# Kernel optimization log

Measured on AMD Instinct MI355X. Metric: run time of the kernel, lower is better.

The kernel has to match this reference:

```python
import jax, jax.numpy as jnp
import numpy as np

DIM = 64
B_GRAPHS = 16
N_NODES = 4096
N_EDGES = 16384
SLOPE = 0.01  # PyTorch leaky_relu default negative slope


def lrelu(x):
    return jnp.where(x >= 0, x, SLOPE * x)


def setup_inputs() -> dict:
    key = jax.random.key(0)
    ks = jax.random.split(key, 16)
    d = DIM

    def rn(k, shape, scale=0.05):
        return jax.random.normal(k, shape, dtype=jnp.float32) * scale

    def z(*s):
        return jnp.zeros(s, jnp.float32)

    return {
        "x": jax.random.normal(ks[0], (N_NODES, 3), dtype=jnp.float32),
        "edge_attr": jax.random.normal(ks[1], (N_EDGES, 4), dtype=jnp.float32),
        "edge_index": jax.random.randint(ks[2], (2, N_EDGES), 0, N_NODES),
        "batch": jnp.sort(jax.random.randint(ks[3], (N_NODES,), 0, B_GRAPHS)),
        # lin0
        "W0": rn(ks[4], (3, d)), "b0": z(d),
        # edge MLP: Linear(4,d) -> LeakyReLU -> Linear(d, d*d)
        "We1": rn(ks[5], (4, d)), "be1": z(d),
        "We2": rn(ks[6], (d, d * d), 0.01), "be2": z(d * d),
        # NNConv root weight + bias
        "root": rn(ks[7], (d, d)), "conv_b": z(d),
        # GRU(d, d)  (PyTorch layout: [3d, in] / [3d, hid], gate order r,z,n)
        "Wih": rn(ks[8], (3 * d, d)), "Whh": rn(ks[9], (3 * d, d)),
        "bih": z(3 * d), "bhh": z(3 * d),
        # Set2Set LSTM(2d, d)  (gate order i,f,g,o)
        "lWih": rn(ks[10], (4 * d, 2 * d)), "lWhh": rn(ks[11], (4 * d, d)),
        "lbih": z(4 * d), "lbhh": z(4 * d),
        # lin_out: Linear(2d, 2)
        "Wout": rn(ks[12], (2 * d, 2)), "bout": z(2),
    }


def _forward(x, edge_attr, W0, b0, We1, be1, We2, be2, root, conv_b,
             Wih, Whh, bih, bhh, lWih, lWhh, lbih, lbhh, Wout, bout,
             edge_index, batch):
    d = DIM
    N = x.shape[0]
    E = edge_attr.shape[0]
    src, dst = edge_index[0], edge_index[1]  # messages flow src(j) -> dst(i)

    out = lrelu(x @ W0 + b0)  # [N, d]
    h = out                    # GRU hidden state (h = out.unsqueeze(0))

    # Edge-conditioned weights: constant across the 6 iterations, compute once.
    he = lrelu(edge_attr @ We1 + be1)          # [E, d]
    W_e = (he @ We2 + be2).reshape(E, d, d)    # [E, d, d]
    deg = jax.ops.segment_sum(jnp.ones((E,), jnp.float32), dst, num_segments=N)
    inv_deg = (1.0 / jnp.maximum(deg, 1.0))[:, None]  # mean aggr, clamp like PyG

    for _ in range(6):
        # NNConv: gather x_j, per-edge matmul, scatter-mean, plus root term
        msg = jnp.einsum('ed,edf->ef', out[src], W_e)            # [E, d]
        agg = jax.ops.segment_sum(msg, dst, num_segments=N) * inv_deg
        m = lrelu(agg + out @ root + conv_b)                     # [N, d]
        # GRU cell (single step, PyTorch gate order r, z, n)
        gi = m @ Wih.T + bih
        gh = h @ Whh.T + bhh
        i_r, i_z, i_n = jnp.split(gi, 3, axis=-1)
        h_r, h_z, h_n = jnp.split(gh, 3, axis=-1)
        r = jax.nn.sigmoid(i_r + h_r)
        zg = jax.nn.sigmoid(i_z + h_z)
        n = jnp.tanh(i_n + r * h_n)
        h = (1.0 - zg) * n + zg * h
        out = h

    # Set2Set pooling, processing_steps = 1
    Bg = B_GRAPHS
    q_star = jnp.zeros((Bg, 2 * d), jnp.float32)
    hl = jnp.zeros((Bg, d), jnp.float32)
    cl = jnp.zeros((Bg, d), jnp.float32)
    gates = q_star @ lWih.T + lbih + hl @ lWhh.T + lbhh
    gi_, gf_, gg_, go_ = jnp.split(gates, 4, axis=-1)
    cl = jax.nn.sigmoid(gf_) * cl + jax.nn.sigmoid(gi_) * jnp.tanh(gg_)
    q = jax.nn.sigmoid(go_) * jnp.tanh(cl)         # [Bg, d]
    e = jnp.sum(out * q[batch], axis=-1)           # [N]
    emax = jax.ops.segment_max(e, batch, num_segments=Bg)
    a = jnp.exp(e - emax[batch])
    asum = jax.ops.segment_sum(a, batch, num_segments=Bg)
    a = a / asum[batch]                            # per-graph softmax attention
    rpool = jax.ops.segment_sum(a[:, None] * out, batch, num_segments=Bg)
    q_star = jnp.concatenate([q, rpool], axis=-1)  # [Bg, 2d]

    return q_star @ Wout + bout                    # [Bg, 2]


def reference(x, edge_attr, edge_index, batch, W0, b0, We1, be1, We2, be2,
              root, conv_b, Wih, Whh, bih, bhh, lWih, lWhh, lbih, lbhh,
              Wout, bout):
    return _forward(x, edge_attr, W0, b0, We1, be1, We2, be2, root, conv_b,
                    Wih, Whh, bih, bhh, lWih, lWhh, lbih, lbhh, Wout, bout,
                    edge_index, batch)
```

## Files before the change

kernel.cpp:

```cpp
#include <hip/hip_runtime.h>
#include <cstddef>

#define NE 16384
#define NN 4096
#define BG 16
#define NT 16
#define ACH 8

__device__ __forceinline__ float lrelu(float v){ return v >= 0.f ? v : 0.01f*v; }
__device__ __forceinline__ float sigm(float v){ return 1.f/(1.f + expf(-v)); }

__global__ __launch_bounds__(256) void setup_kernel(
    const float* __restrict__ x, const float* __restrict__ ea,
    const int* __restrict__ ei,
    const float* __restrict__ W0, const float* __restrict__ b0,
    const float* __restrict__ We1, const float* __restrict__ be1,
    const float* __restrict__ Wih, const float* __restrict__ Whh,
    float* __restrict__ W8T,
    float* __restrict__ h, float* __restrict__ he,
    int* __restrict__ deg, int* __restrict__ cnt)
{
    int t = blockIdx.x*256 + threadIdx.x;
    {
        int e = t >> 6, f = t & 63;
        float v = be1[f];
        #pragma unroll
        for (int d = 0; d < 4; ++d) v += ea[e*4+d]*We1[d*64+f];
        he[t] = lrelu(v);
    }
    if (t < NN*64) {
        int n = t >> 6, f = t & 63;
        float v = b0[f];
        #pragma unroll
        for (int d = 0; d < 3; ++d) v += x[n*3+d]*W0[d*64+f];
        h[t] = lrelu(v);
    }
    if (t < 32768) {
        int k = t >> 9, g = (t >> 3) & 63, j = t & 7;
        float v = 0.f;
        if (j < 3)      v = Wih[(j*64+g)*64 + k];
        else if (j < 6) v = Whh[((j-3)*64+g)*64 + k];
        W8T[t] = v;
    }
    if (t < NE) {
        atomicAdd(&deg[ei[NE + t]], 1);
        atomicAdd(&cnt[ei[t]], 1);
    }
}

__global__ __launch_bounds__(256) void scan_kernel(const int* __restrict__ cnt,
                                                   int* __restrict__ offs)
{
    __shared__ int ps[256];
    int t = threadIdx.x;
    int base = t*16;
    int loc[16];
    int s = 0;
    #pragma unroll
    for (int i = 0; i < 16; ++i) { loc[i] = s; s += cnt[base+i]; }
    ps[t] = s; __syncthreads();
    for (int off = 1; off < 256; off <<= 1) {
        int v = 0;
        if (t >= off) v = ps[t-off];
        __syncthreads();
        if (t >= off) ps[t] += v;
        __syncthreads();
    }
    int pre = (t == 0) ? 0 : ps[t-1];
    #pragma unroll
    for (int i = 0; i < 16; ++i) offs[base+i] = pre + loc[i];
    if (t == 255) offs[NN] = pre + s;
}

__global__ __launch_bounds__(256) void scatter_kernel(
    const int* __restrict__ ei, const int* __restrict__ offs,
    int* __restrict__ cnt,
    int* __restrict__ srcs, int* __restrict__ dsts, int* __restrict__ perm)
{
    int e = blockIdx.x*256 + threadIdx.x;
    if (e >= NE) return;
    int s = ei[e], d = ei[NE + e];
    int old = atomicSub(&cnt[s], 1);
    int pos = offs[s] + old - 1;
    srcs[pos] = s; dsts[pos] = d; perm[pos] = e;
}

__global__ __launch_bounds__(256) void reorder_kernel(
    const float* __restrict__ he, const int* __restrict__ perm,
    float* __restrict__ he_srt)
{
    int t = blockIdx.x*256 + threadIdx.x;
    he_srt[t] = he[(size_t)perm[t>>6]*64 + (t & 63)];
}

__global__ __launch_bounds__(256) void inv_range_kernel(
    const int* __restrict__ deg, const int* __restrict__ batch,
    float* __restrict__ inv_deg, int* __restrict__ gstart, int* __restrict__ gend)
{
    int n = blockIdx.x*256 + threadIdx.x;
    if (n >= NN) return;
    inv_deg[n] = 1.f / fmaxf((float)deg[n], 1.f);
    int b  = batch[n];
    int bp = (n == 0)    ? -1 : batch[n-1];
    int bn = (n == NN-1) ? BG : batch[n+1];
    for (int g = bp+1; g <= b; ++g) gstart[g] = n;
    for (int g = b;   g <  bn; ++g) gend[g]   = n+1;
    if (n == 0)    for (int g = 0;   g < b;  ++g) gend[g]   = 0;
    if (n == NN-1) for (int g = b+1; g < BG; ++g) gstart[g] = NN;
}

__global__ __launch_bounds__(1024) void conv_kernel(
    const float* __restrict__ h, const float* __restrict__ We2,
    const float* __restrict__ be2, const float* __restrict__ he_srt,
    const int* __restrict__ offs, const int* __restrict__ srcs,
    const int* __restrict__ dsts, float* __restrict__ agg)
{
    __shared__ float hsT[64][NT];
    __shared__ float Tb [NT][64];
    __shared__ float Tc [2][ACH][NT][64];
    __shared__ float he_s[2][128][ACH];
    int t  = threadIdx.x;
    int n0 = blockIdx.x * NT;

    { int n = t >> 6, i = t & 63; hsT[i][n] = h[(size_t)(n0+n)*64 + i]; }
    int ebase = offs[n0];
    int ecnt  = offs[n0+NT] - ebase;
    int eend  = ebase + ecnt;
    __syncthreads();

    int aT = t >> 6;
    int nT = ((t >> 4) & 3) * 4;
    int fT = (t & 15) * 4;
    int ct   = t - 512;
    int slot = ct >> 4;
    int f4   = (ct & 15) * 4;
    int nl0=-1,dt0=0,nl1=-1,dt1=0,nl2=-1,dt2=0,nl3=-1,dt3=0;
    float4 m0={0,0,0,0},m1={0,0,0,0},m2={0,0,0,0},m3={0,0,0,0};
    if (t >= 512) {
        if (slot      < ecnt) { nl0 = srcs[ebase+slot]    - n0; dt0 = dsts[ebase+slot];    }
        if (slot + 32 < ecnt) { nl1 = srcs[ebase+slot+32] - n0; dt1 = dsts[ebase+slot+32]; }
        if (slot + 64 < ecnt) { nl2 = srcs[ebase+slot+64] - n0; dt2 = dsts[ebase+slot+64]; }
        if (slot + 96 < ecnt) { nl3 = srcs[ebase+slot+96] - n0; dt3 = dsts[ebase+slot+96]; }
    }

#define EDGE_ACC(mj, nlj, row, buf_) \
    if (nlj >= 0) { \
        float4 hA = *(const float4*)&he_s[buf_][row][0]; \
        float4 hB = *(const float4*)&he_s[buf_][row][4]; \
        float4 t0 = *(const float4*)&Tc[buf_][0][nlj][f4]; \
        float4 t1 = *(const float4*)&Tc[buf_][1][nlj][f4]; \
        float4 t2 = *(const float4*)&Tc[buf_][2][nlj][f4]; \
        float4 t3 = *(const float4*)&Tc[buf_][3][nlj][f4]; \
        float4 t4 = *(const float4*)&Tc[buf_][4][nlj][f4]; \
        float4 t5 = *(const float4*)&Tc[buf_][5][nlj][f4]; \
        float4 t6 = *(const float4*)&Tc[buf_][6][nlj][f4]; \
        float4 t7 = *(const float4*)&Tc[buf_][7][nlj][f4]; \
        mj.x += hA.x*t0.x+hA.y*t1.x+hA.z*t2.x+hA.w*t3.x+hB.x*t4.x+hB.y*t5.x+hB.z*t6.x+hB.w*t7.x; \
        mj.y += hA.x*t0.y+hA.y*t1.y+hA.z*t2.y+hA.w*t3.y+hB.x*t4.y+hB.y*t5.y+hB.z*t6.y+hB.w*t7.y; \
        mj.z += hA.x*t0.z+hA.y*t1.z+hA.z*t2.z+hA.w*t3.z+hB.x*t4.z+hB.y*t5.z+hB.z*t6.z+hB.w*t7.z; \
        mj.w += hA.x*t0.w+hA.y*t1.w+hA.z*t2.w+hA.w*t3.w+hB.x*t4.w+hB.y*t5.w+hB.z*t6.w+hB.w*t7.w; \
    }

#define CONSUME(cm) { \
    int buf_ = (cm) & 1; \
    EDGE_ACC(m0, nl0, (slot),      buf_) \
    EDGE_ACC(m1, nl1, (slot+32),   buf_) \
    EDGE_ACC(m2, nl2, (slot+64),   buf_) \
    EDGE_ACC(m3, nl3, (slot+96),   buf_) \
    for (int e = ebase + 128 + slot; e < eend; e += 32) { \
        int nl = srcs[e] - n0, dtv = dsts[e]; \
        const float* hep = he_srt + (size_t)e*64 + (cm)*ACH; \
        float4 pm = {0,0,0,0}; \
        _Pragma("unroll") \
        for (int a = 0; a < ACH; ++a) { \
            float hv = hep[a]; \
            float4 tv = *(const float4*)&Tc[buf_][a][nl][f4]; \
            pm.x += hv*tv.x; pm.y += hv*tv.y; pm.z += hv*tv.z; pm.w += hv*tv.w; \
        } \
        if ((cm) == 0) { \
            float4 b = *(const float4*)&Tb[nl][f4]; \
            pm.x += b.x; pm.y += b.y; pm.z += b.z; pm.w += b.w; \
        } \
        float* ap = agg + (size_t)dtv*64 + f4; \
        atomicAdd(ap+0, pm.x); atomicAdd(ap+1, pm.y); \
        atomicAdd(ap+2, pm.z); atomicAdd(ap+3, pm.w); \
    } \
}

    for (int c = 0; c < 8; ++c) {
        if (t < 512) {
            const float* Wp = We2 + (size_t)(c*ACH + aT)*4096 + fT;
            float4 A0={0,0,0,0},A1={0,0,0,0},A2={0,0,0,0},A3={0,0,0,0};
            #pragma unroll 8
            for (int i = 0; i < 64; ++i) {
                float4 w  = *(const float4*)(Wp + (size_t)i*64);
                float4 hv = *(const float4*)&hsT[i][nT];
                A0.x += hv.x*w.x; A0.y += hv.x*w.y; A0.z += hv.x*w.z; A0.w += hv.x*w.w;
                A1.x += hv.y*w.x; A1.y += hv.y*w.y; A1.z += hv.y*w.z; A1.w += hv.y*w.w;
                A2.x += hv.z*w.x; A2.y += hv.z*w.y; A2.z += hv.z*w.z; A2.w += hv.z*w.w;
                A3.x += hv.w*w.x; A3.y += hv.w*w.y; A3.z += hv.w*w.z; A3.w += hv.w*w.w;
            }
            int buf = c & 1;
            *(float4*)&Tc[buf][aT][nT+0][fT] = A0;
            *(float4*)&Tc[buf][aT][nT+1][fT] = A1;
            *(float4*)&Tc[buf][aT][nT+2][fT] = A2;
            *(float4*)&Tc[buf][aT][nT+3][fT] = A3;
            if (c == 0) {
                #pragma unroll
                for (int r = 0; r < 2; ++r) {
                    int idx = t + r*512;
                    int n = idx >> 6, f = idx & 63;
                    float acc = 0.f;
                    #pragma unroll 8
                    for (int i = 0; i < 64; ++i) acc += hsT[i][n]*be2[i*64+f];
                    Tb[n][f] = acc;
                }
            }
        } else {
            {
                int le = ct >> 2, a2 = (ct & 3) * 2;
                if (ebase + le < NE)
                    *(float2*)&he_s[c&1][le][a2] =
                        *(const float2*)&he_srt[(size_t)(ebase+le)*64 + c*ACH + a2];
            }
            if (c >= 1) CONSUME(c-1);
        }
        __syncthreads();
    }
    if (t >= 512) {
        CONSUME(7);
        if (nl0 >= 0) {
            float4 b = *(const float4*)&Tb[nl0][f4];
            float* ap = agg + (size_t)dt0*64 + f4;
            atomicAdd(ap+0, m0.x+b.x); atomicAdd(ap+1, m0.y+b.y);
            atomicAdd(ap+2, m0.z+b.z); atomicAdd(ap+3, m0.w+b.w);
        }
        if (nl1 >= 0) {
            float4 b = *(const float4*)&Tb[nl1][f4];
            float* ap = agg + (size_t)dt1*64 + f4;
            atomicAdd(ap+0, m1.x+b.x); atomicAdd(ap+1, m1.y+b.y);
            atomicAdd(ap+2, m1.z+b.z); atomicAdd(ap+3, m1.w+b.w);
        }
        if (nl2 >= 0) {
            float4 b = *(const float4*)&Tb[nl2][f4];
            float* ap = agg + (size_t)dt2*64 + f4;
            atomicAdd(ap+0, m2.x+b.x); atomicAdd(ap+1, m2.y+b.y);
            atomicAdd(ap+2, m2.z+b.z); atomicAdd(ap+3, m2.w+b.w);
        }
        if (nl3 >= 0) {
            float4 b = *(const float4*)&Tb[nl3][f4];
            float* ap = agg + (size_t)dt3*64 + f4;
            atomicAdd(ap+0, m3.x+b.x); atomicAdd(ap+1, m3.y+b.y);
            atomicAdd(ap+2, m3.z+b.z); atomicAdd(ap+3, m3.w+b.w);
        }
    }
#undef CONSUME
#undef EDGE_ACC
}

__global__ __launch_bounds__(512) void node_kernel(
    const float* __restrict__ W8T, const float* __restrict__ root,
    const float* __restrict__ conv_b, const float* __restrict__ inv_deg,
    const float* __restrict__ bih, const float* __restrict__ bhh,
    float* __restrict__ h, float* __restrict__ agg)
{
    __shared__ float hs[8][64];
    __shared__ float ms[8][64];
    int t = threadIdx.x;
    int n = t >> 6, g = t & 63;
    int gn = blockIdx.x*8 + n;
    hs[n][g] = h[(size_t)gn*64 + g];
    __syncthreads();
    {
        size_t ix = (size_t)gn*64 + g;
        float v = agg[ix]*inv_deg[gn] + conv_b[g];
        agg[ix] = 0.f;
        #pragma unroll 8
        for (int k = 0; k < 64; ++k) v += hs[n][k]*root[k*64 + g];
        ms[n][g] = lrelu(v);
    }
    __syncthreads();

    float ir=0.f, iz=0.f, in_=0.f, hr=0.f, hz=0.f, hn=0.f;
    const float* Wp = W8T + (size_t)g*8;
    #pragma unroll 8
    for (int k = 0; k < 64; ++k) {
        float am = ms[n][k], ah = hs[n][k];
        float4 w0 = *(const float4*)(Wp + (size_t)k*512);
        float4 w1 = *(const float4*)(Wp + (size_t)k*512 + 4);
        ir  += am*w0.x; iz += am*w0.y; in_ += am*w0.z;
        hr  += ah*w0.w; hz += ah*w1.x; hn  += ah*w1.y;
    }
    float r  = sigm(ir + bih[g]      + hr + bhh[g]);
    float z  = sigm(iz + bih[64+g]   + hz + bhh[64+g]);
    float nn = tanhf(in_ + bih[128+g] + r*(hn + bhh[128+g]));
    h[(size_t)gn*64 + g] = (1.f - z)*nn + z*hs[n][g];
}

__device__ __forceinline__ float q_val(const float* lbih, const float* lbhh, int g)
{
    float gi = lbih[g]     + lbhh[g];
    float gg = lbih[128+g] + lbhh[128+g];
    float go = lbih[192+g] + lbhh[192+g];
    return sigm(go)*tanhf(sigm(gi)*tanhf(gg));
}

__global__ __launch_bounds__(256) void e_kernel(
    const float* __restrict__ h, const float* __restrict__ lbih,
    const float* __restrict__ lbhh, float* __restrict__ e)
{
    __shared__ float qs[64];
    int t = threadIdx.x;
    if (t < 64) qs[t] = q_val(lbih, lbhh, t);
    __syncthreads();
    int w = t >> 6, f = t & 63;
    int n = blockIdx.x*4 + w;
    float p = h[(size_t)n*64 + f]*qs[f];
    #pragma unroll
    for (int off = 32; off; off >>= 1) p += __shfl_xor(p, off);
    if (f == 0) e[n] = p;
}

__global__ __launch_bounds__(1024) void pool_kernel(
    const float* __restrict__ h, float* __restrict__ e,
    const int* __restrict__ gstart, const int* __restrict__ gend,
    const float* __restrict__ lbih, const float* __restrict__ lbhh,
    const float* __restrict__ Wout, const float* __restrict__ bout,
    float* __restrict__ out)
{
    __shared__ float red[1024];
    __shared__ float rp[64];
    __shared__ float sval;
    int g = blockIdx.x, t = threadIdx.x;
    int s = gstart[g], en = gend[g];

    float mx = -1e30f;
    for (int n = s+t; n < en; n += 1024) mx = fmaxf(mx, e[n]);
    red[t] = mx; __syncthreads();
    for (int st = 512; st; st >>= 1) { if (t < st) red[t] = fmaxf(red[t], red[t+st]); __syncthreads(); }
    if (t == 0) sval = red[0];
    __syncthreads();
    float lmx = sval;
    __syncthreads();

    float sm = 0.f;
    for (int n = s+t; n < en; n += 1024) { float a = expf(e[n]-lmx); e[n] = a; sm += a; }
    red[t] = sm; __syncthreads();
    for (int st = 512; st; st >>= 1) { if (t < st) red[t] += red[t+st]; __syncthreads(); }
    if (t == 0) sval = (red[0] > 0.f) ? 1.f/red[0] : 0.f;
    __syncthreads();
    float inv_asum = sval;
    __syncthreads();

    int w = t >> 6, f = t & 63;
    float racc = 0.f;
    for (int n = s+w; n < en; n += 16) racc += e[n]*h[(size_t)n*64 + f];
    red[t] = racc; __syncthreads();
    if (w == 0) {
        float a = 0.f;
        #pragma unroll
        for (int i = 0; i < 16; ++i) a += red[i*64 + f];
        rp[f] = a*inv_asum;
    }
    __syncthreads();

    if (t < 64) {
        float qv = q_val(lbih, lbhh, t);
        float p0 = qv*Wout[t*2]   + rp[t]*Wout[(64+t)*2];
        float p1 = qv*Wout[t*2+1] + rp[t]*Wout[(64+t)*2+1];
        #pragma unroll
        for (int off = 32; off; off >>= 1) { p0 += __shfl_xor(p0, off); p1 += __shfl_xor(p1, off); }
        if (t == 0) { out[g*2] = p0 + bout[0]; out[g*2+1] = p1 + bout[1]; }
    }
}

extern "C" void kernel_launch(void* const* d_in, const int* in_sizes, int n_in,
                              void* d_out, int out_size, void* d_ws, size_t ws_size,
                              hipStream_t stream)
{
    const float* x      = (const float*)d_in[0];
    const float* ea     = (const float*)d_in[1];
    const int*   ei     = (const int*)  d_in[2];
    const int*   batch  = (const int*)  d_in[3];
    const float* W0     = (const float*)d_in[4];
    const float* b0     = (const float*)d_in[5];
    const float* We1    = (const float*)d_in[6];
    const float* be1    = (const float*)d_in[7];
    const float* We2    = (const float*)d_in[8];
    const float* be2    = (const float*)d_in[9];
    const float* root   = (const float*)d_in[10];
    const float* conv_b = (const float*)d_in[11];
    const float* Wih    = (const float*)d_in[12];
    const float* Whh    = (const float*)d_in[13];
    const float* bih    = (const float*)d_in[14];
    const float* bhh    = (const float*)d_in[15];
    const float* lbih   = (const float*)d_in[18];
    const float* lbhh   = (const float*)d_in[19];
    const float* Wout   = (const float*)d_in[20];
    const float* bout   = (const float*)d_in[21];
    float* out = (float*)d_out;

    float* W = (float*)d_ws;
    size_t off = 0;
    float* h       = W + off; off += (size_t)NN*64;
    float* he      = W + off; off += (size_t)NE*64;
    float* he_srt  = W + off; off += (size_t)NE*64;
    float* agg     = W + off; off += (size_t)NN*64;
    float* W8T     = W + off; off += 32768;
    float* inv_deg = W + off; off += NN;
    float* e       = W + off; off += NN;
    int*   deg     = (int*)(W + off); off += NN;
    int*   cnt     = (int*)(W + off); off += NN;
    int*   offs    = (int*)(W + off); off += NN+1;
    int*   srcs    = (int*)(W + off); off += NE;
    int*   dsts    = (int*)(W + off); off += NE;
    int*   perm    = (int*)(W + off); off += NE;
    int*   gstart  = (int*)(W + off); off += BG;
    int*   gend    = (int*)(W + off); off += BG;

    hipMemsetAsync(deg, 0, 2*NN*sizeof(int), stream);
    hipMemsetAsync(agg, 0, (size_t)NN*64*sizeof(float), stream);
    setup_kernel<<<4096, 256, 0, stream>>>(x, ea, ei, W0, b0, We1, be1, Wih, Whh,
                                           W8T, h, he, deg, cnt);
    scan_kernel<<<1, 256, 0, stream>>>(cnt, offs);
    scatter_kernel<<<64, 256, 0, stream>>>(ei, offs, cnt, srcs, dsts, perm);
    reorder_kernel<<<4096, 256, 0, stream>>>(he, perm, he_srt);
    inv_range_kernel<<<16, 256, 0, stream>>>(deg, batch, inv_deg, gstart, gend);

    for (int it = 0; it < 6; ++it) {
        conv_kernel<<<NN/NT, 1024, 0, stream>>>(h, We2, be2, he_srt,
                                                offs, srcs, dsts, agg);
        node_kernel<<<NN/8, 512, 0, stream>>>(W8T, root, conv_b,
                                              inv_deg, bih, bhh, h, agg);
    }

    e_kernel<<<NN/4, 256, 0, stream>>>(h, lbih, lbhh, e);
    pool_kernel<<<BG, 1024, 0, stream>>>(h, e, gstart, gend, lbih, lbhh, Wout, bout, out);
}
```

Baseline: 558.0 us.

## Fuse conv/GRU iterations and pooling into one cooperative persistent kernel

Replaces the six conv+node launch pairs plus the e/pool kernels with a single cooperative kernel of 256 blocks that uses grid.sync between phases. It keeps h for the block's 16 nodes in shared memory across iterations, double-buffers agg so zeroing happens in the node phase, and preloads each block's edge features into shared memory once. It also merges the inv_range work into the scan kernel. The aim is to remove launch overhead and global round trips. In exchange it relies on all 256 blocks of 1024 threads being co-resident with a larger shared-memory footprint, and grid-wide barriers may cost more than separate launches.

```diff
diff --git a/kernel.cpp b/kernel.cpp
--- a/kernel.cpp
+++ b/kernel.cpp
@@ -1,5 +1,8 @@
 #include <hip/hip_runtime.h>
+#include <hip/hip_cooperative_groups.h>
 #include <cstddef>
+
+namespace cg = cooperative_groups;
 
 #define NE 16384
 #define NN 4096
@@ -9,6 +12,9 @@
 
 __device__ __forceinline__ float lrelu(float v){ return v >= 0.f ? v : 0.01f*v; }
 __device__ __forceinline__ float sigm(float v){ return 1.f/(1.f + expf(-v)); }
+__device__ __forceinline__ void fma4(float4& a, float s, const float4& w){
+    a.x += s*w.x; a.y += s*w.y; a.z += s*w.z; a.w += s*w.w;
+}
 
 __global__ __launch_bounds__(256) void setup_kernel(
     const float* __restrict__ x, const float* __restrict__ ea,
@@ -48,8 +54,10 @@
     }
 }
 
-__global__ __launch_bounds__(256) void scan_kernel(const int* __restrict__ cnt,
-                                                   int* __restrict__ offs)
+__global__ __launch_bounds__(256) void scan_inv_kernel(
+    const int* __restrict__ cnt, int* __restrict__ offs,
+    const int* __restrict__ deg, const int* __restrict__ batch,
+    float* __restrict__ inv_deg, int* __restrict__ gstart, int* __restrict__ gend)
 {
     __shared__ int ps[256];
     int t = threadIdx.x;
@@ -70,6 +78,18 @@
     #pragma unroll
     for (int i = 0; i < 16; ++i) offs[base+i] = pre + loc[i];
     if (t == 255) offs[NN] = pre + s;
+
+    for (int i = 0; i < 16; ++i) {
+        int n = base + i;
+        inv_deg[n] = 1.f / fmaxf((float)deg[n], 1.f);
+        int b  = batch[n];
+        int bp = (n == 0)    ? -1 : batch[n-1];
+        int bn = (n == NN-1) ? BG : batch[n+1];
+        for (int g = bp+1; g <= b; ++g) gstart[g] = n;
+        for (int g = b;   g <  bn; ++g) gend[g]   = n+1;
+        if (n == 0)    for (int g = 0;   g < b;  ++g) gend[g]   = 0;
+        if (n == NN-1) for (int g = b+1; g < BG; ++g) gstart[g] = NN;
+    }
 }
 
 __global__ __launch_bounds__(256) void scatter_kernel(
@@ -93,40 +113,56 @@
     he_srt[t] = he[(size_t)perm[t>>6]*64 + (t & 63)];
 }
 
-__global__ __launch_bounds__(256) void inv_range_kernel(
-    const int* __restrict__ deg, const int* __restrict__ batch,
-    float* __restrict__ inv_deg, int* __restrict__ gstart, int* __restrict__ gend)
-{
-    int n = blockIdx.x*256 + threadIdx.x;
-    if (n >= NN) return;
-    inv_deg[n] = 1.f / fmaxf((float)deg[n], 1.f);
-    int b  = batch[n];
-    int bp = (n == 0)    ? -1 : batch[n-1];
-    int bn = (n == NN-1) ? BG : batch[n+1];
-    for (int g = bp+1; g <= b; ++g) gstart[g] = n;
-    for (int g = b;   g <  bn; ++g) gend[g]   = n+1;
-    if (n == 0)    for (int g = 0;   g < b;  ++g) gend[g]   = 0;
-    if (n == NN-1) for (int g = b+1; g < BG; ++g) gstart[g] = NN;
-}
-
-__global__ __launch_bounds__(1024) void conv_kernel(
-    const float* __restrict__ h, const float* __restrict__ We2,
+__device__ __forceinline__ float q_val(const float* lbih, const float* lbhh, int g)
+{
+    float gi = lbih[g]     + lbhh[g];
+    float gg = lbih[128+g] + lbhh[128+g];
+    float go = lbih[192+g] + lbhh[192+g];
+    return sigm(go)*tanhf(sigm(gi)*tanhf(gg));
+}
+
+__global__ __launch_bounds__(1024) void mega_kernel(
+    float* __restrict__ h, const float* __restrict__ We2,
     const float* __restrict__ be2, const float* __restrict__ he_srt,
     const int* __restrict__ offs, const int* __restrict__ srcs,
-    const int* __restrict__ dsts, float* __restrict__ agg)
+    const int* __restrict__ dsts, float* __restrict__ agg,
+    const float* __restrict__ W8T, const float* __restrict__ root,
+    const float* __restrict__ conv_b, const float* __restrict__ inv_deg,
+    const float* __restrict__ bih, const float* __restrict__ bhh,
+    const int* __restrict__ gstart, const int* __restrict__ gend,
+    const float* __restrict__ lbih, const float* __restrict__ lbhh,
+    const float* __restrict__ Wout, const float* __restrict__ bout,
+    float* __restrict__ ebuf, float* __restrict__ out)
 {
     __shared__ float hsT[64][NT];
     __shared__ float Tb [NT][64];
     __shared__ float Tc [2][ACH][NT][64];
-    __shared__ float he_s[2][128][ACH];
+    __shared__ float he_all[128][72];
+    __shared__ float ms [NT][64];
+    __shared__ float red[1024];
+    __shared__ float qs[64];
+    __shared__ float rp[64];
+    __shared__ float sval;
+
+    cg::grid_group grid = cg::this_grid();
     int t  = threadIdx.x;
     int n0 = blockIdx.x * NT;
-
-    { int n = t >> 6, i = t & 63; hsT[i][n] = h[(size_t)(n0+n)*64 + i]; }
     int ebase = offs[n0];
     int ecnt  = offs[n0+NT] - ebase;
     int eend  = ebase + ecnt;
-    __syncthreads();
+
+    {
+        int n = t >> 6, i = t & 63;
+        hsT[i][n] = h[(size_t)(n0+n)*64 + i];
+    }
+    #pragma unroll
+    for (int r = 0; r < 2; ++r) {
+        int idx = t + r*1024;
+        int sl = idx >> 4, a4 = (idx & 15) * 4;
+        if (ebase + sl < NE)
+            *(float4*)&he_all[sl][a4] =
+                *(const float4*)&he_srt[(size_t)(ebase+sl)*64 + a4];
+    }
 
     int aT = t >> 6;
     int nT = ((t >> 4) & 3) * 4;
@@ -135,243 +171,213 @@
     int slot = ct >> 4;
     int f4   = (ct & 15) * 4;
     int nl0=-1,dt0=0,nl1=-1,dt1=0,nl2=-1,dt2=0,nl3=-1,dt3=0;
-    float4 m0={0,0,0,0},m1={0,0,0,0},m2={0,0,0,0},m3={0,0,0,0};
     if (t >= 512) {
         if (slot      < ecnt) { nl0 = srcs[ebase+slot]    - n0; dt0 = dsts[ebase+slot];    }
         if (slot + 32 < ecnt) { nl1 = srcs[ebase+slot+32] - n0; dt1 = dsts[ebase+slot+32]; }
         if (slot + 64 < ecnt) { nl2 = srcs[ebase+slot+64] - n0; dt2 = dsts[ebase+slot+64]; }
         if (slot + 96 < ecnt) { nl3 = srcs[ebase+slot+96] - n0; dt3 = dsts[ebase+slot+96]; }
     }
-
-#define EDGE_ACC(mj, nlj, row, buf_) \
+    __syncthreads();
+
+#define EDGE_ACC(mj, nlj, row, cm, buf_) \
     if (nlj >= 0) { \
-        float4 hA = *(const float4*)&he_s[buf_][row][0]; \
-        float4 hB = *(const float4*)&he_s[buf_][row][4]; \
-        float4 t0 = *(const float4*)&Tc[buf_][0][nlj][f4]; \
-        float4 t1 = *(const float4*)&Tc[buf_][1][nlj][f4]; \
-        float4 t2 = *(const float4*)&Tc[buf_][2][nlj][f4]; \
-        float4 t3 = *(const float4*)&Tc[buf_][3][nlj][f4]; \
-        float4 t4 = *(const float4*)&Tc[buf_][4][nlj][f4]; \
-        float4 t5 = *(const float4*)&Tc[buf_][5][nlj][f4]; \
-        float4 t6 = *(const float4*)&Tc[buf_][6][nlj][f4]; \
-        float4 t7 = *(const float4*)&Tc[buf_][7][nlj][f4]; \
-        mj.x += hA.x*t0.x+hA.y*t1.x+hA.z*t2.x+hA.w*t3.x+hB.x*t4.x+hB.y*t5.x+hB.z*t6.x+hB.w*t7.x; \
-        mj.y += hA.x*t0.y+hA.y*t1.y+hA.z*t2.y+hA.w*t3.y+hB.x*t4.y+hB.y*t5.y+hB.z*t6.y+hB.w*t7.y; \
-        mj.z += hA.x*t0.z+hA.y*t1.z+hA.z*t2.z+hA.w*t3.z+hB.x*t4.z+hB.y*t5.z+hB.z*t6.z+hB.w*t7.z; \
-        mj.w += hA.x*t0.w+hA.y*t1.w+hA.z*t2.w+hA.w*t3.w+hB.x*t4.w+hB.y*t5.w+hB.z*t6.w+hB.w*t7.w; \
+        float4 hA = *(const float4*)&he_all[row][(cm)*8]; \
+        float4 hB = *(const float4*)&he_all[row][(cm)*8 + 4]; \
+        float he8[8] = {hA.x,hA.y,hA.z,hA.w,hB.x,hB.y,hB.z,hB.w}; \
+        _Pragma("unroll") \
+        for (int a_ = 0; a_ < 8; ++a_) { \
+            float4 tv = *(const float4*)&Tc[buf_][a_][nlj][f4]; \
+            fma4(mj, he8[a_], tv); \
+        } \
     }
 
 #define CONSUME(cm) { \
     int buf_ = (cm) & 1; \
-    EDGE_ACC(m0, nl0, (slot),      buf_) \
-    EDGE_ACC(m1, nl1, (slot+32),   buf_) \
-    EDGE_ACC(m2, nl2, (slot+64),   buf_) \
-    EDGE_ACC(m3, nl3, (slot+96),   buf_) \
+    EDGE_ACC(m0, nl0, (slot),      cm, buf_) \
+    EDGE_ACC(m1, nl1, (slot+32),   cm, buf_) \
+    EDGE_ACC(m2, nl2, (slot+64),   cm, buf_) \
+    EDGE_ACC(m3, nl3, (slot+96),   cm, buf_) \
     for (int e = ebase + 128 + slot; e < eend; e += 32) { \
         int nl = srcs[e] - n0, dtv = dsts[e]; \
         const float* hep = he_srt + (size_t)e*64 + (cm)*ACH; \
         float4 pm = {0,0,0,0}; \
         _Pragma("unroll") \
-        for (int a = 0; a < ACH; ++a) { \
-            float hv = hep[a]; \
-            float4 tv = *(const float4*)&Tc[buf_][a][nl][f4]; \
-            pm.x += hv*tv.x; pm.y += hv*tv.y; pm.z += hv*tv.z; pm.w += hv*tv.w; \
+        for (int a_ = 0; a_ < 8; ++a_) { \
+            float hv = hep[a_]; \
+            float4 tv = *(const float4*)&Tc[buf_][a_][nl][f4]; \
+            fma4(pm, hv, tv); \
         } \
         if ((cm) == 0) { \
             float4 b = *(const float4*)&Tb[nl][f4]; \
             pm.x += b.x; pm.y += b.y; pm.z += b.z; pm.w += b.w; \
         } \
-        float* ap = agg + (size_t)dtv*64 + f4; \
+        float* ap = aggp + (size_t)dtv*64 + f4; \
         atomicAdd(ap+0, pm.x); atomicAdd(ap+1, pm.y); \
         atomicAdd(ap+2, pm.z); atomicAdd(ap+3, pm.w); \
     } \
 }
 
-    for (int c = 0; c < 8; ++c) {
-        if (t < 512) {
-            const float* Wp = We2 + (size_t)(c*ACH + aT)*4096 + fT;
-            float4 A0={0,0,0,0},A1={0,0,0,0},A2={0,0,0,0},A3={0,0,0,0};
+    for (int it = 0; it < 6; ++it) {
+        float* aggp = agg + (size_t)(it & 1) * NN * 64;
+        float4 m0={0,0,0,0},m1={0,0,0,0},m2={0,0,0,0},m3={0,0,0,0};
+
+        for (int c = 0; c < 8; ++c) {
+            if (t < 512) {
+                const float* Wp = We2 + (size_t)(c*ACH + aT)*4096 + fT;
+                float4 A0={0,0,0,0},A1={0,0,0,0},A2={0,0,0,0},A3={0,0,0,0};
+                #pragma unroll 8
+                for (int i = 0; i < 64; ++i) {
+                    float4 w  = *(const float4*)(Wp + (size_t)i*64);
+                    float4 hv = *(const float4*)&hsT[i][nT];
+                    A0.x += hv.x*w.x; A0.y += hv.x*w.y; A0.z += hv.x*w.z; A0.w += hv.x*w.w;
+                    A1.x += hv.y*w.x; A1.y += hv.y*w.y; A1.z += hv.y*w.z; A1.w += hv.y*w.w;
+                    A2.x += hv.z*w.x; A2.y += hv.z*w.y; A2.z += hv.z*w.z; A2.w += hv.z*w.w;
+                    A3.x += hv.w*w.x; A3.y += hv.w*w.y; A3.z += hv.w*w.z; A3.w += hv.w*w.w;
+                }
+                int buf = c & 1;
+                *(float4*)&Tc[buf][aT][nT+0][fT] = A0;
+                *(float4*)&Tc[buf][aT][nT+1][fT] = A1;
+                *(float4*)&Tc[buf][aT][nT+2][fT] = A2;
+                *(float4*)&Tc[buf][aT][nT+3][fT] = A3;
+            } else {
+                if (c == 0) {
+                    int n = ct >> 5, fp = (ct & 31) * 2;
+                    float t0 = 0.f, t1 = 0.f;
+                    #pragma unroll 8
+                    for (int i = 0; i < 64; ++i) {
+                        float hv = hsT[i][n];
+                        float2 b = *(const float2*)&be2[(size_t)i*64 + fp];
+                        t0 += hv*b.x; t1 += hv*b.y;
+                    }
+                    Tb[n][fp]   = t0;
+                    Tb[n][fp+1] = t1;
+                } else {
+                    CONSUME(c-1);
+                }
+            }
+            __syncthreads();
+        }
+        if (t >= 512) {
+            CONSUME(7);
+            if (nl0 >= 0) {
+                float4 b = *(const float4*)&Tb[nl0][f4];
+                float* ap = aggp + (size_t)dt0*64 + f4;
+                atomicAdd(ap+0, m0.x+b.x); atomicAdd(ap+1, m0.y+b.y);
+                atomicAdd(ap+2, m0.z+b.z); atomicAdd(ap+3, m0.w+b.w);
+            }
+            if (nl1 >= 0) {
+                float4 b = *(const float4*)&Tb[nl1][f4];
+                float* ap = aggp + (size_t)dt1*64 + f4;
+                atomicAdd(ap+0, m1.x+b.x); atomicAdd(ap+1, m1.y+b.y);
+                atomicAdd(ap+2, m1.z+b.z); atomicAdd(ap+3, m1.w+b.w);
+            }
+            if (nl2 >= 0) {
+                float4 b = *(const float4*)&Tb[nl2][f4];
+                float* ap = aggp + (size_t)dt2*64 + f4;
+                atomicAdd(ap+0, m2.x+b.x); atomicAdd(ap+1, m2.y+b.y);
+                atomicAdd(ap+2, m2.z+b.z); atomicAdd(ap+3, m2.w+b.w);
+            }
+            if (nl3 >= 0) {
+                float4 b = *(const float4*)&Tb[nl3][f4];
+                float* ap = aggp + (size_t)dt3*64 + f4;
+                atomicAdd(ap+0, m3.x+b.x); atomicAdd(ap+1, m3.y+b.y);
+                atomicAdd(ap+2, m3.z+b.z); atomicAdd(ap+3, m3.w+b.w);
+            }
+        }
+        __threadfence();
+        grid.sync();
+
+        {
+            int n = t >> 6, g = t & 63;
+            int gn = n0 + n;
+            size_t ix = (size_t)gn*64 + g;
+            float v = aggp[ix]*inv_deg[gn] + conv_b[g];
+            aggp[ix] = 0.f;
             #pragma unroll 8
-            for (int i = 0; i < 64; ++i) {
-                float4 w  = *(const float4*)(Wp + (size_t)i*64);
-                float4 hv = *(const float4*)&hsT[i][nT];
-                A0.x += hv.x*w.x; A0.y += hv.x*w.y; A0.z += hv.x*w.z; A0.w += hv.x*w.w;
-                A1.x += hv.y*w.x; A1.y += hv.y*w.y; A1.z += hv.y*w.z; A1.w += hv.y*w.w;
-                A2.x += hv.z*w.x; A2.y += hv.z*w.y; A2.z += hv.z*w.z; A2.w += hv.z*w.w;
-                A3.x += hv.w*w.x; A3.y += hv.w*w.y; A3.z += hv.w*w.z; A3.w += hv.w*w.w;
-            }
-            int buf = c & 1;
-            *(float4*)&Tc[buf][aT][nT+0][fT] = A0;
-            *(float4*)&Tc[buf][aT][nT+1][fT] = A1;
-            *(float4*)&Tc[buf][aT][nT+2][fT] = A2;
-            *(float4*)&Tc[buf][aT][nT+3][fT] = A3;
-            if (c == 0) {
-                #pragma unroll
-                for (int r = 0; r < 2; ++r) {
-                    int idx = t + r*512;
-                    int n = idx >> 6, f = idx & 63;
-                    float acc = 0.f;
-                    #pragma unroll 8
-                    for (int i = 0; i < 64; ++i) acc += hsT[i][n]*be2[i*64+f];
-                    Tb[n][f] = acc;
-                }
-            }
-        } else {
-            {
-                int le = ct >> 2, a2 = (ct & 3) * 2;
-                if (ebase + le < NE)
-                    *(float2*)&he_s[c&1][le][a2] =
-                        *(const float2*)&he_srt[(size_t)(ebase+le)*64 + c*ACH + a2];
-            }
-            if (c >= 1) CONSUME(c-1);
-        }
-        __syncthreads();
-    }
-    if (t >= 512) {
-        CONSUME(7);
-        if (nl0 >= 0) {
-            float4 b = *(const float4*)&Tb[nl0][f4];
-            float* ap = agg + (size_t)dt0*64 + f4;
-            atomicAdd(ap+0, m0.x+b.x); atomicAdd(ap+1, m0.y+b.y);
-            atomicAdd(ap+2, m0.z+b.z); atomicAdd(ap+3, m0.w+b.w);
-        }
-        if (nl1 >= 0) {
-            float4 b = *(const float4*)&Tb[nl1][f4];
-            float* ap = agg + (size_t)dt1*64 + f4;
-            atomicAdd(ap+0, m1.x+b.x); atomicAdd(ap+1, m1.y+b.y);
-            atomicAdd(ap+2, m1.z+b.z); atomicAdd(ap+3, m1.w+b.w);
-        }
-        if (nl2 >= 0) {
-            float4 b = *(const float4*)&Tb[nl2][f4];
-            float* ap = agg + (size_t)dt2*64 + f4;
-            atomicAdd(ap+0, m2.x+b.x); atomicAdd(ap+1, m2.y+b.y);
-            atomicAdd(ap+2, m2.z+b.z); atomicAdd(ap+3, m2.w+b.w);
-        }
-        if (nl3 >= 0) {
-            float4 b = *(const float4*)&Tb[nl3][f4];
-            float* ap = agg + (size_t)dt3*64 + f4;
-            atomicAdd(ap+0, m3.x+b.x); atomicAdd(ap+1, m3.y+b.y);
-            atomicAdd(ap+2, m3.z+b.z); atomicAdd(ap+3, m3.w+b.w);
+            for (int k = 0; k < 64; ++k) v += hsT[k][n]*root[k*64 + g];
+            ms[n][g] = lrelu(v);
+            __syncthreads();
+
+            float ir=0.f, iz=0.f, in_=0.f, hr=0.f, hz=0.f, hn=0.f;
+            const float* Wp = W8T + (size_t)g*8;
+            #pragma unroll 8
+            for (int k = 0; k < 64; ++k) {
+                float am = ms[n][k], ah = hsT[k][n];
+                float4 w0 = *(const float4*)(Wp + (size_t)k*512);
+                float4 w1 = *(const float4*)(Wp + (size_t)k*512 + 4);
+                ir  += am*w0.x; iz += am*w0.y; in_ += am*w0.z;
+                hr  += ah*w0.w; hz += ah*w1.x; hn  += ah*w1.y;
+            }
+            float r  = sigm(ir + bih[g]      + hr + bhh[g]);
+            float z  = sigm(iz + bih[64+g]   + hz + bhh[64+g]);
+            float nn = tanhf(in_ + bih[128+g] + r*(hn + bhh[128+g]));
+            float ho = hsT[g][n];
+            float hnew = (1.f - z)*nn + z*ho;
+            __syncthreads();
+            hsT[g][n] = hnew;
+            h[ix] = hnew;
+            __syncthreads();
+        }
+    }
+
+    __threadfence();
+    grid.sync();
+
+    if (blockIdx.x >= BG) return;
+    {
+        int g = blockIdx.x;
+        int s = gstart[g], en = gend[g];
+        if (t < 64) qs[t] = q_val(lbih, lbhh, t);
+        __syncthreads();
+        int w = t >> 6, f = t & 63;
+        for (int n = s + w; n < en; n += 16) {
+            float p = h[(size_t)n*64 + f]*qs[f];
+            #pragma unroll
+            for (int off = 32; off; off >>= 1) p += __shfl_xor(p, off);
+            if (f == 0) ebuf[n] = p;
+        }
+        __syncthreads();
+
+        float mx = -1e30f;
+        for (int n = s+t; n < en; n += 1024) mx = fmaxf(mx, ebuf[n]);
+        red[t] = mx; __syncthreads();
+        for (int st = 512; st; st >>= 1) { if (t < st) red[t] = fmaxf(red[t], red[t+st]); __syncthreads(); }
+        if (t == 0) sval = red[0];
+        __syncthreads();
+        float lmx = sval;
+        __syncthreads();
+
+        float sm = 0.f;
+        for (int n = s+t; n < en; n += 1024) { float a = expf(ebuf[n]-lmx); ebuf[n] = a; sm += a; }
+        red[t] = sm; __syncthreads();
+        for (int st = 512; st; st >>= 1) { if (t < st) red[t] += red[t+st]; __syncthreads(); }
+        if (t == 0) sval = (red[0] > 0.f) ? 1.f/red[0] : 0.f;
+        __syncthreads();
+        float inv_asum = sval;
+        __syncthreads();
+
+        float racc = 0.f;
+        for (int n = s+w; n < en; n += 16) racc += ebuf[n]*h[(size_t)n*64 + f];
+        red[t] = racc; __syncthreads();
+        if (w == 0) {
+            float a = 0.f;
+            #pragma unroll
+            for (int i = 0; i < 16; ++i) a += red[i*64 + f];
+            rp[f] = a*inv_asum;
+        }
+        __syncthreads();
+
+        if (t < 64) {
+            float qv = qs[t];
+            float p0 = qv*Wout[t*2]   + rp[t]*Wout[(64+t)*2];
+            float p1 = qv*Wout[t*2+1] + rp[t]*Wout[(64+t)*2+1];
+            #pragma unroll
+            for (int off = 32; off; off >>= 1) { p0 += __shfl_xor(p0, off); p1 += __shfl_xor(p1, off); }
+            if (t == 0) { out[g*2] = p0 + bout[0]; out[g*2+1] = p1 + bout[1]; }
         }
     }
 #undef CONSUME
 #undef EDGE_ACC
-}
-
-__global__ __launch_bounds__(512) void node_kernel(
-    const float* __restrict__ W8T, const float* __restrict__ root,
-    const float* __restrict__ conv_b, const float* __restrict__ inv_deg,
-    const float* __restrict__ bih, const float* __restrict__ bhh,
-    float* __restrict__ h, float* __restrict__ agg)
-{
-    __shared__ float hs[8][64];
-    __shared__ float ms[8][64];
-    int t = threadIdx.x;
-    int n = t >> 6, g = t & 63;
-    int gn = blockIdx.x*8 + n;
-    hs[n][g] = h[(size_t)gn*64 + g];
-    __syncthreads();
-    {
-        size_t ix = (size_t)gn*64 + g;
-        float v = agg[ix]*inv_deg[gn] + conv_b[g];
-        agg[ix] = 0.f;
-        #pragma unroll 8
-        for (int k = 0; k < 64; ++k) v += hs[n][k]*root[k*64 + g];
-        ms[n][g] = lrelu(v);
-    }
-    __syncthreads();
-
-    float ir=0.f, iz=0.f, in_=0.f, hr=0.f, hz=0.f, hn=0.f;
-    const float* Wp = W8T + (size_t)g*8;
-    #pragma unroll 8
-    for (int k = 0; k < 64; ++k) {
-        float am = ms[n][k], ah = hs[n][k];
-        float4 w0 = *(const float4*)(Wp + (size_t)k*512);
-        float4 w1 = *(const float4*)(Wp + (size_t)k*512 + 4);
-        ir  += am*w0.x; iz += am*w0.y; in_ += am*w0.z;
-        hr  += ah*w0.w; hz += ah*w1.x; hn  += ah*w1.y;
-    }
-    float r  = sigm(ir + bih[g]      + hr + bhh[g]);
-    float z  = sigm(iz + bih[64+g]   + hz + bhh[64+g]);
-    float nn = tanhf(in_ + bih[128+g] + r*(hn + bhh[128+g]));
-    h[(size_t)gn*64 + g] = (1.f - z)*nn + z*hs[n][g];
-}
-
-__device__ __forceinline__ float q_val(const float* lbih, const float* lbhh, int g)
-{
-    float gi = lbih[g]     + lbhh[g];
-    float gg = lbih[128+g] + lbhh[128+g];
-    float go = lbih[192+g] + lbhh[192+g];
-    return sigm(go)*tanhf(sigm(gi)*tanhf(gg));
-}
-
-__global__ __launch_bounds__(256) void e_kernel(
-    const float* __restrict__ h, const float* __restrict__ lbih,
-    const float* __restrict__ lbhh, float* __restrict__ e)
-{
-    __shared__ float qs[64];
-    int t = threadIdx.x;
-    if (t < 64) qs[t] = q_val(lbih, lbhh, t);
-    __syncthreads();
-    int w = t >> 6, f = t & 63;
-    int n = blockIdx.x*4 + w;
-    float p = h[(size_t)n*64 + f]*qs[f];
-    #pragma unroll
-    for (int off = 32; off; off >>= 1) p += __shfl_xor(p, off);
-    if (f == 0) e[n] = p;
-}
-
-__global__ __launch_bounds__(1024) void pool_kernel(
-    const float* __restrict__ h, float* __restrict__ e,
-    const int* __restrict__ gstart, const int* __restrict__ gend,
-    const float* __restrict__ lbih, const float* __restrict__ lbhh,
-    const float* __restrict__ Wout, const float* __restrict__ bout,
-    float* __restrict__ out)
-{
-    __shared__ float red[1024];
-    __shared__ float rp[64];
-    __shared__ float sval;
-    int g = blockIdx.x, t = threadIdx.x;
-    int s = gstart[g], en = gend[g];
-
-    float mx = -1e30f;
-    for (int n = s+t; n < en; n += 1024) mx = fmaxf(mx, e[n]);
-    red[t] = mx; __syncthreads();
-    for (int st = 512; st; st >>= 1) { if (t < st) red[t] = fmaxf(red[t], red[t+st]); __syncthreads(); }
-    if (t == 0) sval = red[0];
-    __syncthreads();
-    float lmx = sval;
-    __syncthreads();
-
-    float sm = 0.f;
-    for (int n = s+t; n < en; n += 1024) { float a = expf(e[n]-lmx); e[n] = a; sm += a; }
-    red[t] = sm; __syncthreads();
-    for (int st = 512; st; st >>= 1) { if (t < st) red[t] += red[t+st]; __syncthreads(); }
-    if (t == 0) sval = (red[0] > 0.f) ? 1.f/red[0] : 0.f;
-    __syncthreads();
-    float inv_asum = sval;
-    __syncthreads();
-
-    int w = t >> 6, f = t & 63;
-    float racc = 0.f;
-    for (int n = s+w; n < en; n += 16) racc += e[n]*h[(size_t)n*64 + f];
-    red[t] = racc; __syncthreads();
-    if (w == 0) {
-        float a = 0.f;
-        #pragma unroll
-        for (int i = 0; i < 16; ++i) a += red[i*64 + f];
-        rp[f] = a*inv_asum;
-    }
-    __syncthreads();
-
-    if (t < 64) {
-        float qv = q_val(lbih, lbhh, t);
-        float p0 = qv*Wout[t*2]   + rp[t]*Wout[(64+t)*2];
-        float p1 = qv*Wout[t*2+1] + rp[t]*Wout[(64+t)*2+1];
-        #pragma unroll
-        for (int off = 32; off; off >>= 1) { p0 += __shfl_xor(p0, off); p1 += __shfl_xor(p1, off); }
-        if (t == 0) { out[g*2] = p0 + bout[0]; out[g*2+1] = p1 + bout[1]; }
-    }
 }
 
 extern "C" void kernel_launch(void* const* d_in, const int* in_sizes, int n_in,
@@ -405,7 +411,7 @@
     float* h       = W + off; off += (size_t)NN*64;
     float* he      = W + off; off += (size_t)NE*64;
     float* he_srt  = W + off; off += (size_t)NE*64;
-    float* agg     = W + off; off += (size_t)NN*64;
+    float* agg     = W + off; off += (size_t)2*NN*64;
     float* W8T     = W + off; off += 32768;
     float* inv_deg = W + off; off += NN;
     float* e       = W + off; off += NN;
@@ -419,21 +425,22 @@
     int*   gend    = (int*)(W + off); off += BG;
 
     hipMemsetAsync(deg, 0, 2*NN*sizeof(int), stream);
-    hipMemsetAsync(agg, 0, (size_t)NN*64*sizeof(float), stream);
+    hipMemsetAsync(agg, 0, (size_t)2*NN*64*sizeof(float), stream);
     setup_kernel<<<4096, 256, 0, stream>>>(x, ea, ei, W0, b0, We1, be1, Wih, Whh,
                                            W8T, h, he, deg, cnt);
-    scan_kernel<<<1, 256, 0, stream>>>(cnt, offs);
+    scan_inv_kernel<<<1, 256, 0, stream>>>(cnt, offs, deg, batch,
+                                           inv_deg, gstart, gend);
     scatter_kernel<<<64, 256, 0, stream>>>(ei, offs, cnt, srcs, dsts, perm);
     reorder_kernel<<<4096, 256, 0, stream>>>(he, perm, he_srt);
-    inv_range_kernel<<<16, 256, 0, stream>>>(deg, batch, inv_deg, gstart, gend);
-
-    for (int it = 0; it < 6; ++it) {
-        conv_kernel<<<NN/NT, 1024, 0, stream>>>(h, We2, be2, he_srt,
-                                                offs, srcs, dsts, agg);
-        node_kernel<<<NN/8, 512, 0, stream>>>(W8T, root, conv_b,
-                                              inv_deg, bih, bhh, h, agg);
-    }
-
-    e_kernel<<<NN/4, 256, 0, stream>>>(h, lbih, lbhh, e);
-    pool_kernel<<<BG, 1024, 0, stream>>>(h, e, gstart, gend, lbih, lbhh, Wout, bout, out);
-}
+
+    void* params[] = {
+        (void*)&h, (void*)&We2, (void*)&be2, (void*)&he_srt,
+        (void*)&offs, (void*)&srcs, (void*)&dsts, (void*)&agg,
+        (void*)&W8T, (void*)&root, (void*)&conv_b, (void*)&inv_deg,
+        (void*)&bih, (void*)&bhh, (void*)&gstart, (void*)&gend,
+        (void*)&lbih, (void*)&lbhh, (void*)&Wout, (void*)&bout,
+        (void*)&e, (void*)&out
+    };
+    hipLaunchCooperativeKernel((void*)mega_kernel, dim3(256), dim3(1024),
+                               params, 0, stream);
+}
```

Result: slower. 1.394 ms (+149.8%).

## Fuse small setup and attention kernels; move bias transform to consumer warps

Applied to the files above, without the earlier changes.

Folds inv_range into the single-block scan kernel and the e_kernel dot products into pool_kernel, which removes two kernel launches. In conv_kernel, the be2 bias projection Tb is now computed by the otherwise idle consumer threads during chunk 0, not by the producer threads that run the We2 GEMM. This shortens the producers' critical path. The cost is serial per-thread work in the single-block scan and per-graph serialized e computation inside pool.

```diff
diff --git a/kernel.cpp b/kernel.cpp
--- a/kernel.cpp
+++ b/kernel.cpp
@@ -48,8 +48,10 @@
     }
 }
 
-__global__ __launch_bounds__(256) void scan_kernel(const int* __restrict__ cnt,
-                                                   int* __restrict__ offs)
+__global__ __launch_bounds__(256) void scan_inv_kernel(
+    const int* __restrict__ cnt, int* __restrict__ offs,
+    const int* __restrict__ deg, const int* __restrict__ batch,
+    float* __restrict__ inv_deg, int* __restrict__ gstart, int* __restrict__ gend)
 {
     __shared__ int ps[256];
     int t = threadIdx.x;
@@ -70,6 +72,18 @@
     #pragma unroll
     for (int i = 0; i < 16; ++i) offs[base+i] = pre + loc[i];
     if (t == 255) offs[NN] = pre + s;
+
+    for (int i = 0; i < 16; ++i) {
+        int n = base + i;
+        inv_deg[n] = 1.f / fmaxf((float)deg[n], 1.f);
+        int b  = batch[n];
+        int bp = (n == 0)    ? -1 : batch[n-1];
+        int bn = (n == NN-1) ? BG : batch[n+1];
+        for (int g = bp+1; g <= b; ++g) gstart[g] = n;
+        for (int g = b;   g <  bn; ++g) gend[g]   = n+1;
+        if (n == 0)    for (int g = 0;   g < b;  ++g) gend[g]   = 0;
+        if (n == NN-1) for (int g = b+1; g < BG; ++g) gstart[g] = NN;
+    }
 }
 
 __global__ __launch_bounds__(256) void scatter_kernel(
@@ -91,22 +105,6 @@
 {
     int t = blockIdx.x*256 + threadIdx.x;
     he_srt[t] = he[(size_t)perm[t>>6]*64 + (t & 63)];
-}
-
-__global__ __launch_bounds__(256) void inv_range_kernel(
-    const int* __restrict__ deg, const int* __restrict__ batch,
-    float* __restrict__ inv_deg, int* __restrict__ gstart, int* __restrict__ gend)
-{
-    int n = blockIdx.x*256 + threadIdx.x;
-    if (n >= NN) return;
-    inv_deg[n] = 1.f / fmaxf((float)deg[n], 1.f);
-    int b  = batch[n];
-    int bp = (n == 0)    ? -1 : batch[n-1];
-    int bn = (n == NN-1) ? BG : batch[n+1];
-    for (int g = bp+1; g <= b; ++g) gstart[g] = n;
-    for (int g = b;   g <  bn; ++g) gend[g]   = n+1;
-    if (n == 0)    for (int g = 0;   g < b;  ++g) gend[g]   = 0;
-    if (n == NN-1) for (int g = b+1; g < BG; ++g) gstart[g] = NN;
 }
 
 __global__ __launch_bounds__(1024) void conv_kernel(
@@ -205,17 +203,6 @@
             *(float4*)&Tc[buf][aT][nT+1][fT] = A1;
             *(float4*)&Tc[buf][aT][nT+2][fT] = A2;
             *(float4*)&Tc[buf][aT][nT+3][fT] = A3;
-            if (c == 0) {
-                #pragma unroll
-                for (int r = 0; r < 2; ++r) {
-                    int idx = t + r*512;
-                    int n = idx >> 6, f = idx & 63;
-                    float acc = 0.f;
-                    #pragma unroll 8
-                    for (int i = 0; i < 64; ++i) acc += hsT[i][n]*be2[i*64+f];
-                    Tb[n][f] = acc;
-                }
-            }
         } else {
             {
                 int le = ct >> 2, a2 = (ct & 3) * 2;
@@ -223,7 +210,20 @@
                     *(float2*)&he_s[c&1][le][a2] =
                         *(const float2*)&he_srt[(size_t)(ebase+le)*64 + c*ACH + a2];
             }
-            if (c >= 1) CONSUME(c-1);
+            if (c == 0) {
+                int n = ct >> 5, fp = (ct & 31) * 2;
+                float t0 = 0.f, t1 = 0.f;
+                #pragma unroll 8
+                for (int i = 0; i < 64; ++i) {
+                    float hv = hsT[i][n];
+                    float2 b = *(const float2*)&be2[(size_t)i*64 + fp];
+                    t0 += hv*b.x; t1 += hv*b.y;
+                }
+                Tb[n][fp]   = t0;
+                Tb[n][fp+1] = t1;
+            } else {
+                CONSUME(c-1);
+            }
         }
         __syncthreads();
     }
@@ -305,22 +305,6 @@
     return sigm(go)*tanhf(sigm(gi)*tanhf(gg));
 }
 
-__global__ __launch_bounds__(256) void e_kernel(
-    const float* __restrict__ h, const float* __restrict__ lbih,
-    const float* __restrict__ lbhh, float* __restrict__ e)
-{
-    __shared__ float qs[64];
-    int t = threadIdx.x;
-    if (t < 64) qs[t] = q_val(lbih, lbhh, t);
-    __syncthreads();
-    int w = t >> 6, f = t & 63;
-    int n = blockIdx.x*4 + w;
-    float p = h[(size_t)n*64 + f]*qs[f];
-    #pragma unroll
-    for (int off = 32; off; off >>= 1) p += __shfl_xor(p, off);
-    if (f == 0) e[n] = p;
-}
-
 __global__ __launch_bounds__(1024) void pool_kernel(
     const float* __restrict__ h, float* __restrict__ e,
     const int* __restrict__ gstart, const int* __restrict__ gend,
@@ -329,10 +313,22 @@
     float* __restrict__ out)
 {
     __shared__ float red[1024];
+    __shared__ float qs[64];
     __shared__ float rp[64];
     __shared__ float sval;
     int g = blockIdx.x, t = threadIdx.x;
     int s = gstart[g], en = gend[g];
+
+    if (t < 64) qs[t] = q_val(lbih, lbhh, t);
+    __syncthreads();
+    int w = t >> 6, f = t & 63;
+    for (int n = s + w; n < en; n += 16) {
+        float p = h[(size_t)n*64 + f]*qs[f];
+        #pragma unroll
+        for (int off = 32; off; off >>= 1) p += __shfl_xor(p, off);
+        if (f == 0) e[n] = p;
+    }
+    __syncthreads();
 
     float mx = -1e30f;
     for (int n = s+t; n < en; n += 1024) mx = fmaxf(mx, e[n]);
@@ -352,7 +348,6 @@
     float inv_asum = sval;
     __syncthreads();
 
-    int w = t >> 6, f = t & 63;
     float racc = 0.f;
     for (int n = s+w; n < en; n += 16) racc += e[n]*h[(size_t)n*64 + f];
     red[t] = racc; __syncthreads();
@@ -365,7 +360,7 @@
     __syncthreads();
 
     if (t < 64) {
-        float qv = q_val(lbih, lbhh, t);
+        float qv = qs[t];
         float p0 = qv*Wout[t*2]   + rp[t]*Wout[(64+t)*2];
         float p1 = qv*Wout[t*2+1] + rp[t]*Wout[(64+t)*2+1];
         #pragma unroll
@@ -422,10 +417,10 @@
     hipMemsetAsync(agg, 0, (size_t)NN*64*sizeof(float), stream);
     setup_kernel<<<4096, 256, 0, stream>>>(x, ea, ei, W0, b0, We1, be1, Wih, Whh,
                                            W8T, h, he, deg, cnt);
-    scan_kernel<<<1, 256, 0, stream>>>(cnt, offs);
+    scan_inv_kernel<<<1, 256, 0, stream>>>(cnt, offs, deg, batch,
+                                           inv_deg, gstart, gend);
     scatter_kernel<<<64, 256, 0, stream>>>(ei, offs, cnt, srcs, dsts, perm);
     reorder_kernel<<<4096, 256, 0, stream>>>(he, perm, he_srt);
-    inv_range_kernel<<<16, 256, 0, stream>>>(deg, batch, inv_deg, gstart, gend);
 
     for (int it = 0; it < 6; ++it) {
         conv_kernel<<<NN/NT, 1024, 0, stream>>>(h, We2, be2, he_srt,
@@ -434,6 +429,6 @@
                                               inv_deg, bih, bhh, h, agg);
     }
 
-    e_kernel<<<NN/4, 256, 0, stream>>>(h, lbih, lbhh, e);
-    pool_kernel<<<BG, 1024, 0, stream>>>(h, e, gstart, gend, lbih, lbhh, Wout, bout, out);
-}
+    pool_kernel<<<BG, 1024, 0, stream>>>(h, e, gstart, gend, lbih, lbhh,
+                                         Wout, bout, out);
+}
```

New measurement: 588.1 us. 5.4% more time.
